# Performance work log

Hardware: AMD Instinct MI355X
Metric: run time of the kernel (lower is better)

The kernel has to match this reference:

```python
import jax, jax.numpy as jnp
import numpy as np

N = 10000      # atoms
E = 320000     # edges (avg degree 32)
C = 128        # hidden_channels
NB = 32        # num_basis
L = 3          # num_layers
CUT = 5.0      # cutoff
G = 8          # graphs in batch


def setup_inputs() -> dict:
    key = jax.random.key(0)
    ks = jax.random.split(key, 32)
    pos = jax.random.normal(ks[0], (N, 3), dtype=jnp.float32) * 2.0
    z = jax.random.randint(ks[1], (N,), 0, 100)
    row = jax.random.randint(ks[2], (E,), 0, N)
    # avoid self-loops so edge_length > 0
    col = (row + 1 + jax.random.randint(ks[3], (E,), 0, N - 1)) % N
    edge_index = jnp.stack([row, col])
    shifts = jnp.zeros((E, 3), dtype=jnp.float32)
    batch_index = jnp.sort(jax.random.randint(ks[4], (N,), 0, G))
    s = 0.05
    p = lambda k, shape: jax.random.normal(k, shape, dtype=jnp.float32) * s
    return {
        'z': z, 'pos': pos, 'edge_index': edge_index, 'shifts': shifts,
        'batch_index': batch_index,
        'emb': p(ks[5], (100, C)),
        # message blocks (stacked over layers)
        'm_w1': p(ks[6], (L, C, C)), 'm_b1': p(ks[7], (L, C)),
        'm_w2': p(ks[8], (L, C, 3 * C)), 'm_b2': p(ks[9], (L, 3 * C)),
        'f_w': p(ks[10], (L, NB, 3 * C)), 'f_b': p(ks[11], (L, 3 * C)),
        # update blocks
        'u_w': p(ks[12], (L, C, C)), 'v_w': p(ks[13], (L, C, C)),
        'up_w1': p(ks[14], (L, 2 * C, C)), 'up_b1': p(ks[15], (L, C)),
        'up_w2': p(ks[16], (L, C, 3 * C)), 'up_b2': p(ks[17], (L, 3 * C)),
        # readout
        'r_w1': p(ks[18], (C, C // 2)), 'r_b1': p(ks[19], (C // 2,)),
        'r_w2': p(ks[20], (C // 2, 1)), 'r_b2': p(ks[21], (1,)),
    }


def painn_energy(pos, shifts, emb, m_w1, m_b1, m_w2, m_b2, f_w, f_b,
                 u_w, v_w, up_w1, up_b1, up_w2, up_b2,
                 r_w1, r_b1, r_w2, r_b2, z, edge_index, batch_index):
    row, col = edge_index[0], edge_index[1]
    scalar = emb[z]                                  # [N, C]
    vector = jnp.zeros((N, 3, C), dtype=pos.dtype)   # [N, 3, C]

    edge_vec = pos[col] - pos[row] + shifts          # [E, 3]
    edge_len = jnp.sqrt(jnp.sum(edge_vec * edge_vec, axis=-1) + 1e-12)  # [E]
    direction = edge_vec / edge_len[:, None]

    # smooth bump envelope (C-inf, compact support)
    scaled = edge_len / CUT
    inside = scaled < 1.0
    denom = jnp.where(inside, 1.0 - scaled * scaled, 1.0)
    gate = jnp.where(inside, jnp.exp(1.0 - 1.0 / denom), 0.0)  # [E]

    # gaussian radial basis
    centers = jnp.linspace(0.0, CUT, NB)
    gamma = 1.0 / (centers[1] - centers[0]) ** 2
    rbf = jnp.exp(-gamma * (edge_len[:, None] - centers) ** 2)  # [E, NB]
    edge_attr = rbf * gate[:, None]

    for l in range(L):
        # --- message ---
        h = jax.nn.silu(scalar[col] @ m_w1[l] + m_b1[l]) @ m_w2[l] + m_b2[l]  # [E, 3C]
        w = h * (edge_attr @ f_w[l] + f_b[l]) * gate[:, None]
        w1, w2, w3 = jnp.split(w, 3, axis=-1)                                 # each [E, C]
        d_scalar = jax.ops.segment_sum(w1, row, num_segments=N)
        msg_vec = vector[col] * w2[:, None, :] + w3[:, None, :] * direction[:, :, None]  # [E,3,C]
        d_vector = jax.ops.segment_sum(msg_vec, row, num_segments=N)
        scalar = scalar + d_scalar
        vector = vector + d_vector
        # --- update ---
        uv = vector @ u_w[l]                                   # [N, 3, C]
        vv = vector @ v_w[l]
        v_norm = jnp.sqrt(jnp.sum(vv * vv, axis=1) + 1e-8)     # [N, C]
        a = jax.nn.silu(jnp.concatenate([scalar, v_norm], axis=-1) @ up_w1[l] + up_b1[l]) @ up_w2[l] + up_b2[l]
        a1, a2, a3 = jnp.split(a, 3, axis=-1)
        scalar = scalar + a1 + a2 * jnp.sum(uv * vv, axis=1)
        vector = vector + a3[:, None, :] * uv

    e_atom = jax.nn.silu(scalar @ r_w1 + r_b1) @ r_w2 + r_b2   # [N, 1]
    return jax.ops.segment_sum(e_atom, batch_index, num_segments=G)  # [G, 1]


def reference(z, pos, edge_index, shifts, batch_index, emb,
              m_w1, m_b1, m_w2, m_b2, f_w, f_b,
              u_w, v_w, up_w1, up_b1, up_w2, up_b2,
              r_w1, r_b1, r_w2, r_b2):
    return painn_energy(pos, shifts, emb, m_w1, m_b1, m_w2, m_b2, f_w, f_b,
                        u_w, v_w, up_w1, up_b1, up_w2, up_b2,
                        r_w1, r_b1, r_w2, r_b2, z, edge_index, batch_index)
```

## Files before the change

### kernel.cpp

```cpp
#include <hip/hip_runtime.h>
#include <math.h>

#define CUTR 5.0f
#define TL 2048
#define NBASIS 32
#define HSC 16.0f
#define TSC 16.0f
#define VSC 64.0f
#define INV_HT (1.0f / (HSC * TSC))
#define INV_HTV (1.0f / (HSC * TSC * VSC))

typedef __attribute__((ext_vector_type(8))) short bf16x8;
typedef __attribute__((ext_vector_type(4))) float f32x4;
typedef __attribute__((ext_vector_type(2))) float f32x2;

__device__ __forceinline__ float silu_f(float x) { return x / (1.0f + expf(-x)); }
__device__ __forceinline__ ushort f2bf(float x) {
  uint b = __float_as_uint(x);
  uint r = (b + 0x7FFFu + ((b >> 16) & 1u)) >> 16;
  return (ushort)r;
}
__device__ __forceinline__ float bf2f(ushort u) { return __uint_as_float((uint)u << 16); }
__device__ __forceinline__ uchar f2fp8(float x) {
  return (uchar)(__builtin_amdgcn_cvt_pk_fp8_f32(x, 0.0f, 0, false) & 0xff);
}
__device__ __forceinline__ f32x2 fp8pair2f(uint u) {
  return __builtin_amdgcn_cvt_pk_f32_fp8((int)u, false);
}
#define BFLO(u) __uint_as_float((u) << 16)
#define BFHI(u) __uint_as_float((u) & 0xFFFF0000u)

__global__ __launch_bounds__(384) void setup_kernel(
    const int* __restrict__ z, const float* __restrict__ emb, float* __restrict__ scalar,
    ushort* __restrict__ sbf, const float* __restrict__ m_w1, const float* __restrict__ m_w2,
    const float* __restrict__ u_w, const float* __restrict__ v_w,
    const float* __restrict__ up_w1, const float* __restrict__ up_w2,
    const float* __restrict__ r_w1, ushort* __restrict__ wt, const float* __restrict__ f_w,
    const float* __restrict__ f_b, uchar* __restrict__ tab, const float* __restrict__ pos,
    const int* __restrict__ ei, const float* __restrict__ shifts, int* __restrict__ counts,
    int N, int E) {
  __shared__ float fws[NBASIS * 384];
  __shared__ float rbf[8][NBASIS];
  __shared__ float gv[8];
  int tid = threadIdx.x;
  int bi = blockIdx.x;
  const int NB_TABLE = 3 * (TL / 8);
  int nbEmb = (N * 128 + 383) / 384;
  int nbW = (548864 + 383) / 384;
  if (bi < NB_TABLE) {
    int l = bi >> 8, tb = bi & 255;
    for (int i = tid; i < NBASIS * 384; i += 384) fws[i] = f_w[l * NBASIS * 384 + i];
    if (tid < 256) {
      int tt = tid >> 5, k = tid & 31;
      float len = (float)(tb * 8 + tt) * (CUTR / (float)(TL - 1));
      const float gamma = (31.0f / 5.0f) * (31.0f / 5.0f);
      float c = 5.0f * (float)k / 31.0f;
      float d = len - c;
      rbf[tt][k] = expf(-gamma * d * d);
      if (k == 0) {
        float s = len * (1.0f / CUTR);
        gv[tt] = (s < 1.0f) ? expf(1.0f - 1.0f / (1.0f - s * s)) : 0.0f;
      }
    }
    __syncthreads();
    int j = tid % 384;
    float fb = f_b[l * 384 + j];
    for (int tt = 0; tt < 8; ++tt) {
      float acc = 0.0f;
#pragma unroll
      for (int k = 0; k < NBASIS; ++k) acc += rbf[tt][k] * fws[k * 384 + j];
      float g = gv[tt];
      tab[(size_t)l * TL * 384 + (size_t)(tb * 8 + tt) * 384 + j] =
          f2fp8(g * (g * acc + fb) * TSC);
    }
    return;
  }
  bi -= NB_TABLE;
  if (bi < nbEmb) {
    int idx = bi * 384 + tid;
    if (idx >= N * 128) return;
    int n = idx >> 7, j = idx & 127;
    float v = emb[z[n] * 128 + j];
    scalar[idx] = v;
    sbf[idx] = f2bf(v);
    return;
  }
  bi -= nbEmb;
  if (bi < nbW) {
    int idx = bi * 384 + tid;
    if (idx >= 548864) return;
    float v;
    if (idx >= 540672) {
      int t = idx - 540672;
      int n = t >> 7, k = t & 127;
      v = r_w1[k * 64 + n];
    } else {
      int l = idx / 180224, local = idx % 180224;
      if (local < 16384) {
        int n = local >> 7, k = local & 127;
        v = m_w1[l * 16384 + k * 128 + n];
      } else if (local < 65536) {
        int t = local - 16384;
        int n = t >> 7, k = t & 127;
        v = m_w2[l * 49152 + k * 384 + n];
      } else if (local < 98304) {
        int t = local - 65536;
        int n = t >> 7, k = t & 127;
        v = (n < 128) ? u_w[l * 16384 + k * 128 + n] : v_w[l * 16384 + k * 128 + (n - 128)];
      } else if (local < 131072) {
        int t = local - 98304;
        int n = t >> 8, k = t & 255;
        v = up_w1[l * 32768 + k * 128 + n];
      } else {
        int t = local - 131072;
        int n = t >> 7, k = t & 127;
        v = up_w2[l * 49152 + k * 384 + n];
      }
    }
    wt[idx] = f2bf(v);
    return;
  }
  bi -= nbW;
  {
    int e = bi * 384 + tid;
    if (e >= E) return;
    int r = ei[e], c = ei[E + e];
    float dx = pos[c * 3 + 0] - pos[r * 3 + 0] + shifts[e * 3 + 0];
    float dy = pos[c * 3 + 1] - pos[r * 3 + 1] + shifts[e * 3 + 1];
    float dz = pos[c * 3 + 2] - pos[r * 3 + 2] + shifts[e * 3 + 2];
    float len = sqrtf(dx * dx + dy * dy + dz * dz + 1e-12f);
    if (len < CUTR) atomicAdd(&counts[r], 1);
  }
}

__global__ __launch_bounds__(1024) void scan_kernel(const int* __restrict__ counts,
                                                    int* __restrict__ offs,
                                                    int* __restrict__ cursor, int N) {
  __shared__ int sm[1024];
  int tid = threadIdx.x;
  int CH = (N + 1023) / 1024;
  int base = tid * CH;
  int sum = 0;
  for (int i = 0; i < CH; i++) sum += (base + i < N) ? counts[base + i] : 0;
  sm[tid] = sum;
  __syncthreads();
  for (int o = 1; o < 1024; o <<= 1) {
    int v = (tid >= o) ? sm[tid - o] : 0;
    __syncthreads();
    sm[tid] += v;
    __syncthreads();
  }
  int run = sm[tid] - sum;
  for (int i = 0; i < CH; i++) {
    if (base + i < N) {
      offs[base + i] = run;
      cursor[base + i] = run;
      run += counts[base + i];
    }
  }
  if (tid == 1023) offs[N] = sm[1023];
}

__global__ void fill_kernel(const float* __restrict__ pos, const int* __restrict__ ei,
                            const float* __restrict__ shifts, int* __restrict__ cursor,
                            float4* __restrict__ pk, int E) {
  int e = blockIdx.x * 256 + threadIdx.x;
  if (e >= E) return;
  int r = ei[e], c = ei[E + e];
  float dx = pos[c * 3 + 0] - pos[r * 3 + 0] + shifts[e * 3 + 0];
  float dy = pos[c * 3 + 1] - pos[r * 3 + 1] + shifts[e * 3 + 1];
  float dz = pos[c * 3 + 2] - pos[r * 3 + 2] + shifts[e * 3 + 2];
  float len = sqrtf(dx * dx + dy * dy + dz * dz + 1e-12f);
  if (len >= CUTR) return;
  float inv = 1.0f / len;
  float x = len * ((float)(TL - 1) / CUTR);
  int ib = (int)(x + 0.5f);
  if (ib > TL - 1) ib = TL - 1;
  int p = atomicAdd(&cursor[r], 1);
  pk[p] = make_float4(__int_as_float(c | (ib << 14)), dx * inv, dy * inv, dz * inv);
}

__global__ __launch_bounds__(512) void message_kernel(
    const int* __restrict__ offs, const float4* __restrict__ pk, const ushort* __restrict__ hn8,
    const ushort* __restrict__ vb8, const ushort* __restrict__ tab8, float* __restrict__ scalar,
    ushort* __restrict__ sbf, float* __restrict__ vec, ushort* __restrict__ vbout, int N) {
  __shared__ float red[7][64][8];
  int tid = threadIdx.x;
  int lane = tid & 63;
  int s = tid >> 6;
  int n = blockIdx.x;
  int p0 = offs[n], p1 = offs[n + 1];
  float aS0 = 0.f, aS1 = 0.f;
  float aW00 = 0.f, aW01 = 0.f, aW10 = 0.f, aW11 = 0.f, aW20 = 0.f, aW21 = 0.f;
  float aD00 = 0.f, aD01 = 0.f, aD10 = 0.f, aD11 = 0.f, aD20 = 0.f, aD21 = 0.f;
  int p = p0 + s;
  bool hasA = p < p1, hasB = p + 8 < p1;
  float4 cA, cB;
  if (hasA) cA = pk[p];
  if (hasB) cB = pk[p + 8];
  while (hasA) {
    int bitsA = __float_as_int(cA.x);
    int colA = bitsA & 16383, ibA = bitsA >> 14;
    const ushort* hbA = hn8 + (size_t)colA * 192;
    const ushort* vbA = vb8 + (size_t)colA * 192;
    const ushort* tbA = tab8 + (size_t)ibA * 192;
    uint hA1 = hbA[lane], hA2 = hbA[lane + 64], hA3 = hbA[lane + 128];
    uint vA0 = vbA[lane], vA1 = vbA[lane + 64], vA2 = vbA[lane + 128];
    uint tA1 = tbA[lane], tA2 = tbA[lane + 64], tA3 = tbA[lane + 128];
    uint hB1, hB2, hB3, vB0, vB1, vB2, tB1, tB2, tB3;
    float4 dB;
    if (hasB) {
      int bitsB = __float_as_int(cB.x);
      int colB = bitsB & 16383, ibB = bitsB >> 14;
      dB = cB;
      const ushort* hbB = hn8 + (size_t)colB * 192;
      const ushort* vbB = vb8 + (size_t)colB * 192;
      const ushort* tbB = tab8 + (size_t)ibB * 192;
      hB1 = hbB[lane]; hB2 = hbB[lane + 64]; hB3 = hbB[lane + 128];
      vB0 = vbB[lane]; vB1 = vbB[lane + 64]; vB2 = vbB[lane + 128];
      tB1 = tbB[lane]; tB2 = tbB[lane + 64]; tB3 = tbB[lane + 128];
    }
    int pn = p + 16;
    bool nA = pn < p1, nB = pn + 8 < p1;
    float4 fA, fB;
    if (nA) fA = pk[pn];
    if (nB) fB = pk[pn + 8];
    {
      f32x2 dh1 = fp8pair2f(hA1), dh2 = fp8pair2f(hA2), dh3 = fp8pair2f(hA3);
      f32x2 dt1 = fp8pair2f(tA1), dt2 = fp8pair2f(tA2), dt3 = fp8pair2f(tA3);
      f32x2 dv0 = fp8pair2f(vA0), dv1 = fp8pair2f(vA1), dv2 = fp8pair2f(vA2);
      aS0 += dh1.x * dt1.x;
      aS1 += dh1.y * dt1.y;
      float w2l = dh2.x * dt2.x, w2h = dh2.y * dt2.y;
      float w3l = dh3.x * dt3.x, w3h = dh3.y * dt3.y;
      aW00 += dv0.x * w2l; aW01 += dv0.y * w2h;
      aW10 += dv1.x * w2l; aW11 += dv1.y * w2h;
      aW20 += dv2.x * w2l; aW21 += dv2.y * w2h;
      aD00 += w3l * cA.y; aD01 += w3h * cA.y;
      aD10 += w3l * cA.z; aD11 += w3h * cA.z;
      aD20 += w3l * cA.w; aD21 += w3h * cA.w;
    }
    if (hasB) {
      f32x2 dh1 = fp8pair2f(hB1), dh2 = fp8pair2f(hB2), dh3 = fp8pair2f(hB3);
      f32x2 dt1 = fp8pair2f(tB1), dt2 = fp8pair2f(tB2), dt3 = fp8pair2f(tB3);
      f32x2 dv0 = fp8pair2f(vB0), dv1 = fp8pair2f(vB1), dv2 = fp8pair2f(vB2);
      aS0 += dh1.x * dt1.x;
      aS1 += dh1.y * dt1.y;
      float w2l = dh2.x * dt2.x, w2h = dh2.y * dt2.y;
      float w3l = dh3.x * dt3.x, w3h = dh3.y * dt3.y;
      aW00 += dv0.x * w2l; aW01 += dv0.y * w2h;
      aW10 += dv1.x * w2l; aW11 += dv1.y * w2h;
      aW20 += dv2.x * w2l; aW21 += dv2.y * w2h;
      aD00 += w3l * dB.y; aD01 += w3h * dB.y;
      aD10 += w3l * dB.z; aD11 += w3h * dB.z;
      aD20 += w3l * dB.w; aD21 += w3h * dB.w;
    }
    cA = fA;
    cB = fB;
    hasA = nA;
    hasB = nB;
    p = pn;
  }
  float sS0 = aS0 * INV_HT, sS1 = aS1 * INV_HT;
  float sV00 = aW00 * INV_HTV + aD00 * INV_HT;
  float sV01 = aW01 * INV_HTV + aD01 * INV_HT;
  float sV10 = aW10 * INV_HTV + aD10 * INV_HT;
  float sV11 = aW11 * INV_HTV + aD11 * INV_HT;
  float sV20 = aW20 * INV_HTV + aD20 * INV_HT;
  float sV21 = aW21 * INV_HTV + aD21 * INV_HT;
  if (s) {
    float* r = &red[s - 1][lane][0];
    r[0] = sS0; r[1] = sS1;
    r[2] = sV00; r[3] = sV01;
    r[4] = sV10; r[5] = sV11;
    r[6] = sV20; r[7] = sV21;
  }
  __syncthreads();
  if (s == 0) {
#pragma unroll
    for (int q = 0; q < 7; ++q) {
      const float* r = &red[q][lane][0];
      sS0 += r[0]; sS1 += r[1];
      sV00 += r[2]; sV01 += r[3];
      sV10 += r[4]; sV11 += r[5];
      sV20 += r[6]; sV21 += r[7];
    }
    float2* sp = (float2*)(scalar + (size_t)n * 128) + lane;
    float2 sv = *sp;
    sv.x += sS0;
    sv.y += sS1;
    *sp = sv;
    ((uint*)(sbf + (size_t)n * 128))[lane] = (uint)f2bf(sv.x) | ((uint)f2bf(sv.y) << 16);
    float2* vp0 = (float2*)(vec + (size_t)n * 384) + lane;
    float2* vp1 = (float2*)(vec + (size_t)n * 384 + 128) + lane;
    float2* vp2 = (float2*)(vec + (size_t)n * 384 + 256) + lane;
    float2 v0 = *vp0, v1 = *vp1, v2 = *vp2;
    v0.x += sV00; v0.y += sV01;
    v1.x += sV10; v1.y += sV11;
    v2.x += sV20; v2.y += sV21;
    *vp0 = v0; *vp1 = v1; *vp2 = v2;
    uint* ob = (uint*)(vbout + (size_t)n * 384);
    ob[lane] = (uint)f2bf(v0.x) | ((uint)f2bf(v0.y) << 16);
    ob[lane + 64] = (uint)f2bf(v1.x) | ((uint)f2bf(v1.y) << 16);
    ob[lane + 128] = (uint)f2bf(v2.x) | ((uint)f2bf(v2.y) << 16);
  }
}

__global__ __launch_bounds__(512) void mlp_kernel(const ushort* __restrict__ A,
                                                  const ushort* __restrict__ W1T,
                                                  const float* __restrict__ b1,
                                                  const ushort* __restrict__ W2T,
                                                  const float* __restrict__ b2,
                                                  uchar* __restrict__ out, int M) {
  __shared__ ushort As[32 * 128];
  __shared__ ushort Bs[128 * 128];
  __shared__ ushort Hs[32 * 128];
  int tid = threadIdx.x;
  int lane = tid & 63, w = tid >> 6;
  int mh = w >> 2, wc = w & 3;
  int m0 = blockIdx.x * 32;
  int cl = lane & 15, rq = lane >> 4;
  int ra = mh * 16 + cl;
  f32x4 acc[2] = {};
  {
    {
      int row = tid >> 4, ch = tid & 15;
      uint4 av = make_uint4(0, 0, 0, 0);
      if (m0 + row < M) av = *(const uint4*)(A + (size_t)(m0 + row) * 128 + ch * 8);
      *(uint4*)(&As[row * 128 + ((ch ^ (row & 7)) * 8)]) = av;
    }
#pragma unroll
    for (int r = 0; r < 4; ++r) {
      int c = tid + r * 512;
      int row = c >> 4, ch = c & 15;
      uint4 bv = *(const uint4*)(W1T + (size_t)row * 128 + ch * 8);
      *(uint4*)(&Bs[row * 128 + ((ch ^ (row & 7)) * 8)]) = bv;
    }
    __syncthreads();
#pragma unroll
    for (int ks = 0; ks < 4; ++ks) {
      int ch = ks * 4 + rq;
      bf16x8 a = *(bf16x8*)&As[ra * 128 + ((ch ^ (ra & 7)) * 8)];
#pragma unroll
      for (int ns = 0; ns < 2; ++ns) {
        int rb = wc * 32 + ns * 16 + cl;
        bf16x8 b = *(bf16x8*)&Bs[rb * 128 + ((ch ^ (rb & 7)) * 8)];
        acc[ns] = __builtin_amdgcn_mfma_f32_16x16x32_bf16(a, b, acc[ns], 0, 0, 0);
      }
    }
  }
#pragma unroll
  for (int ns = 0; ns < 2; ++ns) {
    int hcol = wc * 32 + ns * 16 + cl;
    float bv = b1[hcol];
    int chunk = hcol >> 3, el = hcol & 7;
#pragma unroll
    for (int j = 0; j < 4; ++j) {
      int hr = mh * 16 + rq * 4 + j;
      float v = silu_f(acc[ns][j] + bv);
      Hs[hr * 128 + ((chunk ^ (hr & 7)) * 8) + el] = f2bf(v);
    }
  }
  __syncthreads();
  for (int nt = 0; nt < 3; ++nt) {
#pragma unroll
    for (int r = 0; r < 4; ++r) {
      int c = tid + r * 512;
      int row = c >> 4, ch = c & 15;
      uint4 bv = *(const uint4*)(W2T + (size_t)(nt * 128 + row) * 128 + ch * 8);
      *(uint4*)(&Bs[row * 128 + ((ch ^ (row & 7)) * 8)]) = bv;
    }
    __syncthreads();
    f32x4 acc2[2] = {};
#pragma unroll
    for (int ks = 0; ks < 4; ++ks) {
      int ch = ks * 4 + rq;
      bf16x8 a = *(bf16x8*)&Hs[ra * 128 + ((ch ^ (ra & 7)) * 8)];
#pragma unroll
      for (int ns = 0; ns < 2; ++ns) {
        int rb = wc * 32 + ns * 16 + cl;
        bf16x8 b = *(bf16x8*)&Bs[rb * 128 + ((ch ^ (rb & 7)) * 8)];
        acc2[ns] = __builtin_amdgcn_mfma_f32_16x16x32_bf16(a, b, acc2[ns], 0, 0, 0);
      }
    }
#pragma unroll
    for (int ns = 0; ns < 2; ++ns) {
      int col = nt * 128 + wc * 32 + ns * 16 + cl;
      float bv = b2[col];
#pragma unroll
      for (int j = 0; j < 4; ++j) {
        int m = m0 + mh * 16 + rq * 4 + j;
        if (m >= M) continue;
        out[(size_t)m * 384 + col] = f2fp8((acc2[ns][j] + bv) * HSC);
      }
    }
    __syncthreads();
  }
}

__global__ __launch_bounds__(512) void mlp2_kernel(const ushort* __restrict__ sbf_in,
                                                   const ushort* __restrict__ W1T,
                                                   const float* __restrict__ b1,
                                                   const ushort* __restrict__ W2T,
                                                   const float* __restrict__ b2,
                                                   const ushort* __restrict__ uvvv,
                                                   float* __restrict__ scalar,
                                                   ushort* __restrict__ sbf,
                                                   float* __restrict__ vec,
                                                   uchar* __restrict__ vbf8, int M) {
  __shared__ ushort As[32 * 128];
  __shared__ ushort Bs[128 * 128];
  __shared__ ushort Hs[32 * 128];
  int tid = threadIdx.x;
  int lane = tid & 63, w = tid >> 6;
  int mh = w >> 2, wc = w & 3;
  int m0 = blockIdx.x * 32;
  int cl = lane & 15, rq = lane >> 4;
  int ra = mh * 16 + cl;
  f32x4 acc[2] = {};
  for (int k0 = 0; k0 < 256; k0 += 128) {
    __syncthreads();
    {
      int row = tid >> 4, ch = tid & 15;
      uint4 av = make_uint4(0, 0, 0, 0);
      if (m0 + row < M) {
        if (k0 == 0) {
          av = *(const uint4*)(sbf_in + (size_t)(m0 + row) * 128 + ch * 8);
        } else {
          const ushort* ub = uvvv + (size_t)(m0 + row) * 768 + 128 + ch * 8;
          bf16x8 x0 = *(const bf16x8*)(ub);
          bf16x8 x1 = *(const bf16x8*)(ub + 256);
          bf16x8 x2 = *(const bf16x8*)(ub + 512);
          ushort pkv[8];
#pragma unroll
          for (int e = 0; e < 8; ++e) {
            float a = bf2f((ushort)x0[e]), bb = bf2f((ushort)x1[e]), cc = bf2f((ushort)x2[e]);
            pkv[e] = f2bf(sqrtf(a * a + bb * bb + cc * cc + 1e-8f));
          }
          av = *(uint4*)pkv;
        }
      }
      *(uint4*)(&As[row * 128 + ((ch ^ (row & 7)) * 8)]) = av;
    }
#pragma unroll
    for (int r = 0; r < 4; ++r) {
      int c = tid + r * 512;
      int row = c >> 4, ch = c & 15;
      uint4 bv = *(const uint4*)(W1T + (size_t)row * 256 + k0 + ch * 8);
      *(uint4*)(&Bs[row * 128 + ((ch ^ (row & 7)) * 8)]) = bv;
    }
    __syncthreads();
#pragma unroll
    for (int ks = 0; ks < 4; ++ks) {
      int ch = ks * 4 + rq;
      bf16x8 a = *(bf16x8*)&As[ra * 128 + ((ch ^ (ra & 7)) * 8)];
#pragma unroll
      for (int ns = 0; ns < 2; ++ns) {
        int rb = wc * 32 + ns * 16 + cl;
        bf16x8 b = *(bf16x8*)&Bs[rb * 128 + ((ch ^ (rb & 7)) * 8)];
        acc[ns] = __builtin_amdgcn_mfma_f32_16x16x32_bf16(a, b, acc[ns], 0, 0, 0);
      }
    }
  }
#pragma unroll
  for (int ns = 0; ns < 2; ++ns) {
    int hcol = wc * 32 + ns * 16 + cl;
    float bv = b1[hcol];
    int chunk = hcol >> 3, el = hcol & 7;
#pragma unroll
    for (int j = 0; j < 4; ++j) {
      int hr = mh * 16 + rq * 4 + j;
      float v = silu_f(acc[ns][j] + bv);
      Hs[hr * 128 + ((chunk ^ (hr & 7)) * 8) + el] = f2bf(v);
    }
  }
  __syncthreads();
  f32x4 aReg[3][2];
  for (int nt = 0; nt < 3; ++nt) {
#pragma unroll
    for (int r = 0; r < 4; ++r) {
      int c = tid + r * 512;
      int row = c >> 4, ch = c & 15;
      uint4 bv = *(const uint4*)(W2T + (size_t)(nt * 128 + row) * 128 + ch * 8);
      *(uint4*)(&Bs[row * 128 + ((ch ^ (row & 7)) * 8)]) = bv;
    }
    __syncthreads();
    f32x4 acc2[2] = {};
#pragma unroll
    for (int ks = 0; ks < 4; ++ks) {
      int ch = ks * 4 + rq;
      bf16x8 a = *(bf16x8*)&Hs[ra * 128 + ((ch ^ (ra & 7)) * 8)];
#pragma unroll
      for (int ns = 0; ns < 2; ++ns) {
        int rb = wc * 32 + ns * 16 + cl;
        bf16x8 b = *(bf16x8*)&Bs[rb * 128 + ((ch ^ (rb & 7)) * 8)];
        acc2[ns] = __builtin_amdgcn_mfma_f32_16x16x32_bf16(a, b, acc2[ns], 0, 0, 0);
      }
    }
#pragma unroll
    for (int ns = 0; ns < 2; ++ns) aReg[nt][ns] = acc2[ns];
    __syncthreads();
  }
#pragma unroll
  for (int ns = 0; ns < 2; ++ns) {
    int chOff = wc * 32 + ns * 16 + cl;
    float b2a = b2[chOff], b2b = b2[128 + chOff], b2c = b2[256 + chOff];
#pragma unroll
    for (int j = 0; j < 4; ++j) {
      int nn = m0 + mh * 16 + rq * 4 + j;
      if (nn >= M) continue;
      float a1 = aReg[0][ns][j] + b2a;
      float a2 = aReg[1][ns][j] + b2b;
      float a3 = aReg[2][ns][j] + b2c;
      const ushort* ub = uvvv + (size_t)nn * 768;
      float uv0 = bf2f(ub[chOff]), vv0 = bf2f(ub[128 + chOff]);
      float uv1 = bf2f(ub[256 + chOff]), vv1 = bf2f(ub[384 + chOff]);
      float uv2 = bf2f(ub[512 + chOff]), vv2 = bf2f(ub[640 + chOff]);
      float dot = uv0 * vv0 + uv1 * vv1 + uv2 * vv2;
      size_t si = (size_t)nn * 128 + chOff;
      float s = scalar[si] + a1 + a2 * dot;
      scalar[si] = s;
      sbf[si] = f2bf(s);
      size_t vb = (size_t)nn * 384 + chOff;
      float nv0 = vec[vb] + a3 * uv0;
      float nv1 = vec[vb + 128] + a3 * uv1;
      float nv2 = vec[vb + 256] + a3 * uv2;
      vec[vb] = nv0;
      vec[vb + 128] = nv1;
      vec[vb + 256] = nv2;
      vbf8[vb] = f2fp8(nv0 * VSC);
      vbf8[vb + 128] = f2fp8(nv1 * VSC);
      vbf8[vb + 256] = f2fp8(nv2 * VSC);
    }
  }
}

__global__ __launch_bounds__(256) void gemm_kernel(const ushort* __restrict__ A,
                                                   const ushort* __restrict__ WT,
                                                   ushort* __restrict__ Cout, int M, int K,
                                                   int Nn) {
  __shared__ ushort As[64 * 128];
  __shared__ ushort Bs[64 * 128];
  int tid = threadIdx.x;
  int m0 = blockIdx.x * 64, n0 = blockIdx.y * 64;
  int lane = tid & 63, w = tid >> 6, wr = w >> 1, wc = w & 1;
  f32x4 acc[2][2] = {};
  for (int k0 = 0; k0 < K; k0 += 128) {
    __syncthreads();
#pragma unroll
    for (int r = 0; r < 4; ++r) {
      int c = tid + r * 256;
      int row = c >> 4, col16 = c & 15;
      uint4 av = make_uint4(0, 0, 0, 0);
      if (m0 + row < M) av = *(const uint4*)(A + (size_t)(m0 + row) * K + k0 + col16 * 8);
      *(uint4*)(&As[row * 128 + ((col16 ^ (row & 7)) * 8)]) = av;
      uint4 bv = *(const uint4*)(WT + (size_t)(n0 + row) * K + k0 + col16 * 8);
      *(uint4*)(&Bs[row * 128 + ((col16 ^ (row & 7)) * 8)]) = bv;
    }
    __syncthreads();
#pragma unroll
    for (int ks = 0; ks < 4; ++ks) {
      int ch = ks * 4 + (lane >> 4);
      int ra0 = wr * 32 + (lane & 15), ra1 = ra0 + 16;
      int rb0 = wc * 32 + (lane & 15), rb1 = rb0 + 16;
      bf16x8 a0 = *(bf16x8*)&As[ra0 * 128 + ((ch ^ (ra0 & 7)) * 8)];
      bf16x8 a1 = *(bf16x8*)&As[ra1 * 128 + ((ch ^ (ra1 & 7)) * 8)];
      bf16x8 b0 = *(bf16x8*)&Bs[rb0 * 128 + ((ch ^ (rb0 & 7)) * 8)];
      bf16x8 b1 = *(bf16x8*)&Bs[rb1 * 128 + ((ch ^ (rb1 & 7)) * 8)];
      acc[0][0] = __builtin_amdgcn_mfma_f32_16x16x32_bf16(a0, b0, acc[0][0], 0, 0, 0);
      acc[0][1] = __builtin_amdgcn_mfma_f32_16x16x32_bf16(a0, b1, acc[0][1], 0, 0, 0);
      acc[1][0] = __builtin_amdgcn_mfma_f32_16x16x32_bf16(a1, b0, acc[1][0], 0, 0, 0);
      acc[1][1] = __builtin_amdgcn_mfma_f32_16x16x32_bf16(a1, b1, acc[1][1], 0, 0, 0);
    }
  }
  int cl = lane & 15, rq = lane >> 4;
#pragma unroll
  for (int ms = 0; ms < 2; ++ms)
#pragma unroll
    for (int ns = 0; ns < 2; ++ns) {
      int n = n0 + wc * 32 + ns * 16 + cl;
#pragma unroll
      for (int j = 0; j < 4; ++j) {
        int m = m0 + wr * 32 + ms * 16 + rq * 4 + j;
        if (m >= M) continue;
        Cout[(size_t)m * Nn + n] = f2bf(acc[ms][ns][j]);
      }
    }
}

__global__ __launch_bounds__(256) void readout_kernel(
    const ushort* __restrict__ sbf, const ushort* __restrict__ r1T, const float* __restrict__ rb1,
    const float* __restrict__ r_w2, const float* __restrict__ r_b2, const int* __restrict__ bidx,
    float* __restrict__ out, int N, int G) {
  __shared__ ushort As[64 * 128];
  __shared__ ushort Bs[64 * 128];
  __shared__ float rs[64];
  __shared__ float sm[64];
  int tid = threadIdx.x;
  int m0 = blockIdx.x * 64;
  int lane = tid & 63, w = tid >> 6, wr = w >> 1, wc = w & 1;
  int cl = lane & 15, rq = lane >> 4;
#pragma unroll
  for (int r = 0; r < 4; ++r) {
    int c = tid + r * 256;
    int row = c >> 4, ch = c & 15;
    uint4 av = make_uint4(0, 0, 0, 0);
    if (m0 + row < N) av = *(const uint4*)(sbf + (size_t)(m0 + row) * 128 + ch * 8);
    *(uint4*)(&As[row * 128 + ((ch ^ (row & 7)) * 8)]) = av;
    uint4 bv = *(const uint4*)(r1T + (size_t)row * 128 + ch * 8);
    *(uint4*)(&Bs[row * 128 + ((ch ^ (row & 7)) * 8)]) = bv;
  }
  if (tid < 64) {
    rs[tid] = 0.f;
    sm[tid] = 0.f;
  }
  __syncthreads();
  f32x4 acc[2][2] = {};
#pragma unroll
  for (int ks = 0; ks < 4; ++ks) {
    int ch = ks * 4 + rq;
    int ra0 = wr * 32 + cl, ra1 = ra0 + 16;
    int rb0 = wc * 32 + cl, rb1 = rb0 + 16;
    bf16x8 a0 = *(bf16x8*)&As[ra0 * 128 + ((ch ^ (ra0 & 7)) * 8)];
    bf16x8 a1 = *(bf16x8*)&As[ra1 * 128 + ((ch ^ (ra1 & 7)) * 8)];
    bf16x8 b0 = *(bf16x8*)&Bs[rb0 * 128 + ((ch ^ (rb0 & 7)) * 8)];
    bf16x8 b1 = *(bf16x8*)&Bs[rb1 * 128 + ((ch ^ (rb1 & 7)) * 8)];
    acc[0][0] = __builtin_amdgcn_mfma_f32_16x16x32_bf16(a0, b0, acc[0][0], 0, 0, 0);
    acc[0][1] = __builtin_amdgcn_mfma_f32_16x16x32_bf16(a0, b1, acc[0][1], 0, 0, 0);
    acc[1][0] = __builtin_amdgcn_mfma_f32_16x16x32_bf16(a1, b0, acc[1][0], 0, 0, 0);
    acc[1][1] = __builtin_amdgcn_mfma_f32_16x16x32_bf16(a1, b1, acc[1][1], 0, 0, 0);
  }
#pragma unroll
  for (int ms = 0; ms < 2; ++ms) {
    float part0 = 0.f, part1 = 0.f, part2 = 0.f, part3 = 0.f;
#pragma unroll
    for (int ns = 0; ns < 2; ++ns) {
      int col = wc * 32 + ns * 16 + cl;
      float b1v = rb1[col], wv = r_w2[col];
      part0 += silu_f(acc[ms][ns][0] + b1v) * wv;
      part1 += silu_f(acc[ms][ns][1] + b1v) * wv;
      part2 += silu_f(acc[ms][ns][2] + b1v) * wv;
      part3 += silu_f(acc[ms][ns][3] + b1v) * wv;
    }
#pragma unroll
    for (int o = 1; o < 16; o <<= 1) {
      part0 += __shfl_xor(part0, o);
      part1 += __shfl_xor(part1, o);
      part2 += __shfl_xor(part2, o);
      part3 += __shfl_xor(part3, o);
    }
    if (cl == 0) {
      int rbase = wr * 32 + ms * 16 + rq * 4;
      atomicAdd(&rs[rbase + 0], part0);
      atomicAdd(&rs[rbase + 1], part1);
      atomicAdd(&rs[rbase + 2], part2);
      atomicAdd(&rs[rbase + 3], part3);
    }
  }
  __syncthreads();
  float rb2 = r_b2[0];
  if (tid < 64) {
    int m = m0 + tid;
    if (m < N) atomicAdd(&sm[bidx[m]], rs[tid] + rb2);
  }
  __syncthreads();
  if (tid < G && G <= 64) atomicAdd(&out[tid], sm[tid]);
}

extern "C" void kernel_launch(void* const* d_in, const int* in_sizes, int n_in, void* d_out,
                              int out_size, void* d_ws, size_t ws_size, hipStream_t stream) {
  const int N = in_sizes[0];
  const int E = in_sizes[2] / 2;
  const int G = out_size;

  const int* z = (const int*)d_in[0];
  const float* pos = (const float*)d_in[1];
  const int* ei = (const int*)d_in[2];
  const float* shifts = (const float*)d_in[3];
  const int* bidx = (const int*)d_in[4];
  const float* emb = (const float*)d_in[5];
  const float* m_w1 = (const float*)d_in[6];
  const float* m_b1 = (const float*)d_in[7];
  const float* m_w2 = (const float*)d_in[8];
  const float* m_b2 = (const float*)d_in[9];
  const float* f_w = (const float*)d_in[10];
  const float* f_b = (const float*)d_in[11];
  const float* u_w = (const float*)d_in[12];
  const float* v_w = (const float*)d_in[13];
  const float* up_w1 = (const float*)d_in[14];
  const float* up_b1 = (const float*)d_in[15];
  const float* up_w2 = (const float*)d_in[16];
  const float* up_b2 = (const float*)d_in[17];
  const float* r_w1 = (const float*)d_in[18];
  const float* r_b1 = (const float*)d_in[19];
  const float* r_w2 = (const float*)d_in[20];
  const float* r_b2 = (const float*)d_in[21];
  float* out = (float*)d_out;

  float* w = (float*)d_ws;
  size_t off = 0;
  auto alloc = [&](size_t nfl) { float* p = w + off; off += (nfl + 3) & ~(size_t)3; return p; };
  uchar* tab8 = (uchar*)alloc((size_t)3 * TL * 96);
  float* scalar = alloc((size_t)N * 128);
  ushort* sbf = (ushort*)alloc((size_t)N * 64);
  float* vec = alloc((size_t)N * 384);
  uchar* mir8 = (uchar*)alloc((size_t)N * 96);
  ushort* mir_bf = (ushort*)alloc((size_t)N * 192);
  uchar* hn8 = (uchar*)alloc((size_t)N * 96);
  ushort* uvvv = (ushort*)alloc((size_t)N * 384);
  float* pkf = alloc((size_t)E * 4);
  ushort* wt = (ushort*)alloc((size_t)274432);
  int* counts = (int*)alloc((size_t)N);
  int* offs = (int*)alloc((size_t)N + 4);
  int* cursor = (int*)alloc((size_t)N);
  if (off * sizeof(float) > ws_size) return;

  hipMemsetAsync(counts, 0, (size_t)N * sizeof(int), stream);
  hipMemsetAsync(vec, 0, (size_t)N * 384 * sizeof(float), stream);
  hipMemsetAsync(mir8, 0, (size_t)N * 384, stream);
  hipMemsetAsync(out, 0, (size_t)G * sizeof(float), stream);

  int nbTable = 3 * (TL / 8);
  int nbEmb = (N * 128 + 383) / 384;
  int nbW = (548864 + 383) / 384;
  int nbCount = (E + 383) / 384;
  setup_kernel<<<nbTable + nbEmb + nbW + nbCount, 384, 0, stream>>>(
      z, emb, scalar, sbf, m_w1, m_w2, u_w, v_w, up_w1, up_w2, r_w1, wt, f_w, f_b, tab8, pos, ei,
      shifts, counts, N, E);
  scan_kernel<<<1, 1024, 0, stream>>>(counts, offs, cursor, N);
  fill_kernel<<<(E + 255) / 256, 256, 0, stream>>>(pos, ei, shifts, cursor, (float4*)pkf, E);

  dim3 gm((N + 31) / 32);
  dim3 g3((3 * N + 63) / 64, 4);

  for (int l = 0; l < 3; l++) {
    const ushort* wl = wt + (size_t)l * 180224;
    mlp_kernel<<<gm, 512, 0, stream>>>(sbf, wl, m_b1 + l * 128, wl + 16384, m_b2 + l * 384,
                                       hn8, N);
    message_kernel<<<N, 512, 0, stream>>>(offs, (const float4*)pkf, (const ushort*)hn8,
                                          (const ushort*)mir8,
                                          (const ushort*)(tab8 + (size_t)l * TL * 384), scalar,
                                          sbf, vec, mir_bf, N);
    gemm_kernel<<<g3, 256, 0, stream>>>(mir_bf, wl + 65536, uvvv, 3 * N, 128, 256);
    mlp2_kernel<<<gm, 512, 0, stream>>>(sbf, wl + 98304, up_b1 + l * 128, wl + 131072,
                                        up_b2 + l * 384, uvvv, scalar, sbf, vec, mir8, N);
  }

  readout_kernel<<<(N + 63) / 64, 256, 0, stream>>>(sbf, wt + 540672, r_b1, r_w2, r_b2, bidx,
                                                    out, N, G);
}
```

Measured before the change: 359.0 us.

## Interleave fp8 node and filter tables and use one wave per node in message pass

Node features (h and vector parts) are packed into a single interleaved 768-byte fp8 row per atom, and the radial filter table is padded to 512-byte rows with the same interleaving. Each lane then fetches its channel pair with one 12-byte and one 8-byte load instead of nine scattered 2-byte loads. The message kernel is also restructured from 8 waves per node with a shared-memory reduction to one wave per node with 4 nodes per block, which removes the LDS reduction and the barrier but lowers per-node parallelism for high-degree nodes.

Result: faster. 336.3 us (-6.3%).

```diff
diff --git a/kernel.cpp b/kernel.cpp
--- a/kernel.cpp
+++ b/kernel.cpp
@@ -14,6 +14,8 @@
 typedef __attribute__((ext_vector_type(4))) float f32x4;
 typedef __attribute__((ext_vector_type(2))) float f32x2;
 
+struct U3 { uint x, y, z; };
+
 __device__ __forceinline__ float silu_f(float x) { return x / (1.0f + expf(-x)); }
 __device__ __forceinline__ ushort f2bf(float x) {
   uint b = __float_as_uint(x);
@@ -24,11 +26,12 @@
 __device__ __forceinline__ uchar f2fp8(float x) {
   return (uchar)(__builtin_amdgcn_cvt_pk_fp8_f32(x, 0.0f, 0, false) & 0xff);
 }
-__device__ __forceinline__ f32x2 fp8pair2f(uint u) {
+__device__ __forceinline__ f32x2 fp8lo(uint u) {
   return __builtin_amdgcn_cvt_pk_f32_fp8((int)u, false);
 }
-#define BFLO(u) __uint_as_float((u) << 16)
-#define BFHI(u) __uint_as_float((u) & 0xFFFF0000u)
+__device__ __forceinline__ f32x2 fp8hi(uint u) {
+  return __builtin_amdgcn_cvt_pk_f32_fp8((int)u, true);
+}
 
 __global__ __launch_bounds__(384) void setup_kernel(
     const int* __restrict__ z, const float* __restrict__ emb, float* __restrict__ scalar,
@@ -64,13 +67,14 @@
     }
     __syncthreads();
     int j = tid % 384;
+    int b = j >> 7, ch = j & 127;
     float fb = f_b[l * 384 + j];
     for (int tt = 0; tt < 8; ++tt) {
       float acc = 0.0f;
 #pragma unroll
       for (int k = 0; k < NBASIS; ++k) acc += rbf[tt][k] * fws[k * 384 + j];
       float g = gv[tt];
-      tab[(size_t)l * TL * 384 + (size_t)(tb * 8 + tt) * 384 + j] =
+      tab[((size_t)l * TL + (size_t)(tb * 8 + tt)) * 512 + (ch >> 1) * 8 + b * 2 + (ch & 1)] =
           f2fp8(g * (g * acc + fb) * TSC);
     }
     return;
@@ -180,77 +184,70 @@
   pk[p] = make_float4(__int_as_float(c | (ib << 14)), dx * inv, dy * inv, dz * inv);
 }
 
-__global__ __launch_bounds__(512) void message_kernel(
-    const int* __restrict__ offs, const float4* __restrict__ pk, const ushort* __restrict__ hn8,
-    const ushort* __restrict__ vb8, const ushort* __restrict__ tab8, float* __restrict__ scalar,
-    ushort* __restrict__ sbf, float* __restrict__ vec, ushort* __restrict__ vbout, int N) {
-  __shared__ float red[7][64][8];
-  int tid = threadIdx.x;
-  int lane = tid & 63;
-  int s = tid >> 6;
-  int n = blockIdx.x;
+__global__ __launch_bounds__(256) void message_kernel(
+    const int* __restrict__ offs, const float4* __restrict__ pk, const uchar* __restrict__ hv8,
+    const uchar* __restrict__ tab8, float* __restrict__ scalar, ushort* __restrict__ sbf,
+    float* __restrict__ vec, ushort* __restrict__ vbout, int N) {
+  int lane = threadIdx.x & 63;
+  int n = blockIdx.x * 4 + (threadIdx.x >> 6);
+  if (n >= N) return;
   int p0 = offs[n], p1 = offs[n + 1];
   float aS0 = 0.f, aS1 = 0.f;
   float aW00 = 0.f, aW01 = 0.f, aW10 = 0.f, aW11 = 0.f, aW20 = 0.f, aW21 = 0.f;
   float aD00 = 0.f, aD01 = 0.f, aD10 = 0.f, aD11 = 0.f, aD20 = 0.f, aD21 = 0.f;
-  int p = p0 + s;
-  bool hasA = p < p1, hasB = p + 8 < p1;
+  int p = p0;
+  bool hasA = p < p1, hasB = p + 1 < p1;
   float4 cA, cB;
   if (hasA) cA = pk[p];
-  if (hasB) cB = pk[p + 8];
+  if (hasB) cB = pk[p + 1];
   while (hasA) {
     int bitsA = __float_as_int(cA.x);
     int colA = bitsA & 16383, ibA = bitsA >> 14;
-    const ushort* hbA = hn8 + (size_t)colA * 192;
-    const ushort* vbA = vb8 + (size_t)colA * 192;
-    const ushort* tbA = tab8 + (size_t)ibA * 192;
-    uint hA1 = hbA[lane], hA2 = hbA[lane + 64], hA3 = hbA[lane + 128];
-    uint vA0 = vbA[lane], vA1 = vbA[lane + 64], vA2 = vbA[lane + 128];
-    uint tA1 = tbA[lane], tA2 = tbA[lane + 64], tA3 = tbA[lane + 128];
-    uint hB1, hB2, hB3, vB0, vB1, vB2, tB1, tB2, tB3;
+    U3 hvA = *(const U3*)(hv8 + (size_t)colA * 768 + lane * 12);
+    uint2 tA = *(const uint2*)(tab8 + (size_t)ibA * 512 + lane * 8);
+    U3 hvB;
+    uint2 tB;
     float4 dB;
     if (hasB) {
       int bitsB = __float_as_int(cB.x);
       int colB = bitsB & 16383, ibB = bitsB >> 14;
       dB = cB;
-      const ushort* hbB = hn8 + (size_t)colB * 192;
-      const ushort* vbB = vb8 + (size_t)colB * 192;
-      const ushort* tbB = tab8 + (size_t)ibB * 192;
-      hB1 = hbB[lane]; hB2 = hbB[lane + 64]; hB3 = hbB[lane + 128];
-      vB0 = vbB[lane]; vB1 = vbB[lane + 64]; vB2 = vbB[lane + 128];
-      tB1 = tbB[lane]; tB2 = tbB[lane + 64]; tB3 = tbB[lane + 128];
-    }
-    int pn = p + 16;
-    bool nA = pn < p1, nB = pn + 8 < p1;
+      hvB = *(const U3*)(hv8 + (size_t)colB * 768 + lane * 12);
+      tB = *(const uint2*)(tab8 + (size_t)ibB * 512 + lane * 8);
+    }
+    int pn = p + 2;
+    bool nA = pn < p1, nB = pn + 1 < p1;
     float4 fA, fB;
     if (nA) fA = pk[pn];
-    if (nB) fB = pk[pn + 8];
+    if (nB) fB = pk[pn + 1];
     {
-      f32x2 dh1 = fp8pair2f(hA1), dh2 = fp8pair2f(hA2), dh3 = fp8pair2f(hA3);
-      f32x2 dt1 = fp8pair2f(tA1), dt2 = fp8pair2f(tA2), dt3 = fp8pair2f(tA3);
-      f32x2 dv0 = fp8pair2f(vA0), dv1 = fp8pair2f(vA1), dv2 = fp8pair2f(vA2);
-      aS0 += dh1.x * dt1.x;
-      aS1 += dh1.y * dt1.y;
-      float w2l = dh2.x * dt2.x, w2h = dh2.y * dt2.y;
-      float w3l = dh3.x * dt3.x, w3h = dh3.y * dt3.y;
-      aW00 += dv0.x * w2l; aW01 += dv0.y * w2h;
-      aW10 += dv1.x * w2l; aW11 += dv1.y * w2h;
-      aW20 += dv2.x * w2l; aW21 += dv2.y * w2h;
+      f32x2 h1 = fp8lo(hvA.x), h2 = fp8hi(hvA.x);
+      f32x2 h3 = fp8lo(hvA.y), v0 = fp8hi(hvA.y);
+      f32x2 v1 = fp8lo(hvA.z), v2 = fp8hi(hvA.z);
+      f32x2 t1 = fp8lo(tA.x), t2 = fp8hi(tA.x), t3 = fp8lo(tA.y);
+      aS0 += h1.x * t1.x;
+      aS1 += h1.y * t1.y;
+      float w2l = h2.x * t2.x, w2h = h2.y * t2.y;
+      float w3l = h3.x * t3.x, w3h = h3.y * t3.y;
+      aW00 += v0.x * w2l; aW01 += v0.y * w2h;
+      aW10 += v1.x * w2l; aW11 += v1.y * w2h;
+      aW20 += v2.x * w2l; aW21 += v2.y * w2h;
       aD00 += w3l * cA.y; aD01 += w3h * cA.y;
       aD10 += w3l * cA.z; aD11 += w3h * cA.z;
       aD20 += w3l * cA.w; aD21 += w3h * cA.w;
     }
     if (hasB) {
-      f32x2 dh1 = fp8pair2f(hB1), dh2 = fp8pair2f(hB2), dh3 = fp8pair2f(hB3);
-      f32x2 dt1 = fp8pair2f(tB1), dt2 = fp8pair2f(tB2), dt3 = fp8pair2f(tB3);
-      f32x2 dv0 = fp8pair2f(vB0), dv1 = fp8pair2f(vB1), dv2 = fp8pair2f(vB2);
-      aS0 += dh1.x * dt1.x;
-      aS1 += dh1.y * dt1.y;
-      float w2l = dh2.x * dt2.x, w2h = dh2.y * dt2.y;
-      float w3l = dh3.x * dt3.x, w3h = dh3.y * dt3.y;
-      aW00 += dv0.x * w2l; aW01 += dv0.y * w2h;
-      aW10 += dv1.x * w2l; aW11 += dv1.y * w2h;
-      aW20 += dv2.x * w2l; aW21 += dv2.y * w2h;
+      f32x2 h1 = fp8lo(hvB.x), h2 = fp8hi(hvB.x);
+      f32x2 h3 = fp8lo(hvB.y), v0 = fp8hi(hvB.y);
+      f32x2 v1 = fp8lo(hvB.z), v2 = fp8hi(hvB.z);
+      f32x2 t1 = fp8lo(tB.x), t2 = fp8hi(tB.x), t3 = fp8lo(tB.y);
+      aS0 += h1.x * t1.x;
+      aS1 += h1.y * t1.y;
+      float w2l = h2.x * t2.x, w2h = h2.y * t2.y;
+      float w3l = h3.x * t3.x, w3h = h3.y * t3.y;
+      aW00 += v0.x * w2l; aW01 += v0.y * w2h;
+      aW10 += v1.x * w2l; aW11 += v1.y * w2h;
+      aW20 += v2.x * w2l; aW21 += v2.y * w2h;
       aD00 += w3l * dB.y; aD01 += w3h * dB.y;
       aD10 += w3l * dB.z; aD11 += w3h * dB.z;
       aD20 += w3l * dB.w; aD21 += w3h * dB.w;
@@ -268,42 +265,24 @@
   float sV11 = aW11 * INV_HTV + aD11 * INV_HT;
   float sV20 = aW20 * INV_HTV + aD20 * INV_HT;
   float sV21 = aW21 * INV_HTV + aD21 * INV_HT;
-  if (s) {
-    float* r = &red[s - 1][lane][0];
-    r[0] = sS0; r[1] = sS1;
-    r[2] = sV00; r[3] = sV01;
-    r[4] = sV10; r[5] = sV11;
-    r[6] = sV20; r[7] = sV21;
-  }
-  __syncthreads();
-  if (s == 0) {
-#pragma unroll
-    for (int q = 0; q < 7; ++q) {
-      const float* r = &red[q][lane][0];
-      sS0 += r[0]; sS1 += r[1];
-      sV00 += r[2]; sV01 += r[3];
-      sV10 += r[4]; sV11 += r[5];
-      sV20 += r[6]; sV21 += r[7];
-    }
-    float2* sp = (float2*)(scalar + (size_t)n * 128) + lane;
-    float2 sv = *sp;
-    sv.x += sS0;
-    sv.y += sS1;
-    *sp = sv;
-    ((uint*)(sbf + (size_t)n * 128))[lane] = (uint)f2bf(sv.x) | ((uint)f2bf(sv.y) << 16);
-    float2* vp0 = (float2*)(vec + (size_t)n * 384) + lane;
-    float2* vp1 = (float2*)(vec + (size_t)n * 384 + 128) + lane;
-    float2* vp2 = (float2*)(vec + (size_t)n * 384 + 256) + lane;
-    float2 v0 = *vp0, v1 = *vp1, v2 = *vp2;
-    v0.x += sV00; v0.y += sV01;
-    v1.x += sV10; v1.y += sV11;
-    v2.x += sV20; v2.y += sV21;
-    *vp0 = v0; *vp1 = v1; *vp2 = v2;
-    uint* ob = (uint*)(vbout + (size_t)n * 384);
-    ob[lane] = (uint)f2bf(v0.x) | ((uint)f2bf(v0.y) << 16);
-    ob[lane + 64] = (uint)f2bf(v1.x) | ((uint)f2bf(v1.y) << 16);
-    ob[lane + 128] = (uint)f2bf(v2.x) | ((uint)f2bf(v2.y) << 16);
-  }
+  float2* sp = (float2*)(scalar + (size_t)n * 128) + lane;
+  float2 sv = *sp;
+  sv.x += sS0;
+  sv.y += sS1;
+  *sp = sv;
+  ((uint*)(sbf + (size_t)n * 128))[lane] = (uint)f2bf(sv.x) | ((uint)f2bf(sv.y) << 16);
+  float2* vp0 = (float2*)(vec + (size_t)n * 384) + lane;
+  float2* vp1 = (float2*)(vec + (size_t)n * 384 + 128) + lane;
+  float2* vp2 = (float2*)(vec + (size_t)n * 384 + 256) + lane;
+  float2 v0 = *vp0, v1 = *vp1, v2 = *vp2;
+  v0.x += sV00; v0.y += sV01;
+  v1.x += sV10; v1.y += sV11;
+  v2.x += sV20; v2.y += sV21;
+  *vp0 = v0; *vp1 = v1; *vp2 = v2;
+  uint* ob = (uint*)(vbout + (size_t)n * 384);
+  ob[lane] = (uint)f2bf(v0.x) | ((uint)f2bf(v0.y) << 16);
+  ob[lane + 64] = (uint)f2bf(v1.x) | ((uint)f2bf(v1.y) << 16);
+  ob[lane + 128] = (uint)f2bf(v2.x) | ((uint)f2bf(v2.y) << 16);
 }
 
 __global__ __launch_bounds__(512) void mlp_kernel(const ushort* __restrict__ A,
@@ -385,13 +364,14 @@
     }
 #pragma unroll
     for (int ns = 0; ns < 2; ++ns) {
-      int col = nt * 128 + wc * 32 + ns * 16 + cl;
-      float bv = b2[col];
+      int ch = wc * 32 + ns * 16 + cl;
+      float bv = b2[nt * 128 + ch];
 #pragma unroll
       for (int j = 0; j < 4; ++j) {
         int m = m0 + mh * 16 + rq * 4 + j;
         if (m >= M) continue;
-        out[(size_t)m * 384 + col] = f2fp8((acc2[ns][j] + bv) * HSC);
+        out[(size_t)m * 768 + (ch >> 1) * 12 + nt * 2 + (ch & 1)] =
+            f2fp8((acc2[ns][j] + bv) * HSC);
       }
     }
     __syncthreads();
@@ -528,9 +508,10 @@
       vec[vb] = nv0;
       vec[vb + 128] = nv1;
       vec[vb + 256] = nv2;
-      vbf8[vb] = f2fp8(nv0 * VSC);
-      vbf8[vb + 128] = f2fp8(nv1 * VSC);
-      vbf8[vb + 256] = f2fp8(nv2 * VSC);
+      size_t hb = (size_t)nn * 768 + (chOff >> 1) * 12 + 6 + (chOff & 1);
+      vbf8[hb] = f2fp8(nv0 * VSC);
+      vbf8[hb + 2] = f2fp8(nv1 * VSC);
+      vbf8[hb + 4] = f2fp8(nv2 * VSC);
     }
   }
 }
@@ -700,13 +681,12 @@
   float* w = (float*)d_ws;
   size_t off = 0;
   auto alloc = [&](size_t nfl) { float* p = w + off; off += (nfl + 3) & ~(size_t)3; return p; };
-  uchar* tab8 = (uchar*)alloc((size_t)3 * TL * 96);
+  uchar* tab8 = (uchar*)alloc((size_t)3 * TL * 128);
   float* scalar = alloc((size_t)N * 128);
   ushort* sbf = (ushort*)alloc((size_t)N * 64);
   float* vec = alloc((size_t)N * 384);
-  uchar* mir8 = (uchar*)alloc((size_t)N * 96);
+  uchar* hv8 = (uchar*)alloc((size_t)N * 192);
   ushort* mir_bf = (ushort*)alloc((size_t)N * 192);
-  uchar* hn8 = (uchar*)alloc((size_t)N * 96);
   ushort* uvvv = (ushort*)alloc((size_t)N * 384);
   float* pkf = alloc((size_t)E * 4);
   ushort* wt = (ushort*)alloc((size_t)274432);
@@ -717,7 +697,7 @@
 
   hipMemsetAsync(counts, 0, (size_t)N * sizeof(int), stream);
   hipMemsetAsync(vec, 0, (size_t)N * 384 * sizeof(float), stream);
-  hipMemsetAsync(mir8, 0, (size_t)N * 384, stream);
+  hipMemsetAsync(hv8, 0, (size_t)N * 768, stream);
   hipMemsetAsync(out, 0, (size_t)G * sizeof(float), stream);
 
   int nbTable = 3 * (TL / 8);
@@ -736,14 +716,12 @@
   for (int l = 0; l < 3; l++) {
     const ushort* wl = wt + (size_t)l * 180224;
     mlp_kernel<<<gm, 512, 0, stream>>>(sbf, wl, m_b1 + l * 128, wl + 16384, m_b2 + l * 384,
-                                       hn8, N);
-    message_kernel<<<N, 512, 0, stream>>>(offs, (const float4*)pkf, (const ushort*)hn8,
-                                          (const ushort*)mir8,
-                                          (const ushort*)(tab8 + (size_t)l * TL * 384), scalar,
-                                          sbf, vec, mir_bf, N);
+                                       hv8, N);
+    message_kernel<<<(N + 3) / 4, 256, 0, stream>>>(
+        offs, (const float4*)pkf, hv8, tab8 + (size_t)l * TL * 512, scalar, sbf, vec, mir_bf, N);
     gemm_kernel<<<g3, 256, 0, stream>>>(mir_bf, wl + 65536, uvvv, 3 * N, 128, 256);
     mlp2_kernel<<<gm, 512, 0, stream>>>(sbf, wl + 98304, up_b1 + l * 128, wl + 131072,
-                                        up_b2 + l * 384, uvvv, scalar, sbf, vec, mir8, N);
+                                        up_b2 + l * 384, uvvv, scalar, sbf, vec, hv8, N);
   }
 
   readout_kernel<<<(N + 63) / 64, 256, 0, stream>>>(sbf, wt + 540672, r_b1, r_w2, r_b2, bidx,
```
